# Performance work log

Hardware: AMD Instinct MI355X
Metric: run time of the kernel (lower is better)

Reference implementation:

```python
import jax, jax.numpy as jnp
import numpy as np

B, L, IN_DIM, D, H, NCONV = 64, 400, 500, 128, 8, 4
HD = D // H  # head dim = 16


def _conv1d(x, w, b, pad, groups=1):
    # x: [B, L, Cin], w: [k, Cin//groups, Cout]
    y = jax.lax.conv_general_dilated(
        x, w, window_strides=(1,), padding=[(pad, pad)],
        dimension_numbers=('NWC', 'WIO', 'NWC'), feature_group_count=groups)
    return y + b


def _layernorm(x, g, b, eps=1e-5):
    mu = jnp.mean(x, axis=-1, keepdims=True)
    var = jnp.mean(jnp.square(x - mu), axis=-1, keepdims=True)
    return (x - mu) * jax.lax.rsqrt(var + eps) * g + b


def _posenc(L, d):
    pos = jnp.arange(L, dtype=jnp.float32)[:, None]                 # [L,1]
    div = jnp.exp(jnp.arange(0, d, 2, dtype=jnp.float32) * (-jnp.log(10000.0) / d))
    ang = pos * div                                                 # [L, d/2]
    return jnp.stack([jnp.sin(ang), jnp.cos(ang)], axis=-1).reshape(L, d)


def setup_inputs() -> dict:
    key = jax.random.key(0)
    ks = jax.random.split(key, 24)
    s = lambda k, shape, scale: jax.random.normal(k, shape, dtype=jnp.float32) * scale
    inp = {
        'x': s(ks[0], (B, L, IN_DIM), 1.0),
        # init conv: k=5, 500 -> 128
        'w_init': s(ks[1], (5, IN_DIM, D), 0.02),
        'b_init': jnp.zeros((D,), jnp.float32),
        # 4 depthwise-separable conv layers (pre-LN, residual): depthwise k=7
        'ln_conv_g': jnp.ones((NCONV, D), jnp.float32),
        'ln_conv_b': jnp.zeros((NCONV, D), jnp.float32),
        'w_dw': s(ks[2], (NCONV, 7, 1, D), 0.1),
        'b_dw': jnp.zeros((NCONV, D), jnp.float32),
        'w_pw': s(ks[3], (NCONV, 1, D, D), 0.05),
        'b_pw': jnp.zeros((NCONV, D), jnp.float32),
        # self-attention (pre-LN, residual)
        'ln_att_g': jnp.ones((D,), jnp.float32),
        'ln_att_b': jnp.zeros((D,), jnp.float32),
        'wq': s(ks[4], (D, D), 0.05), 'bq': jnp.zeros((D,), jnp.float32),
        'wk': s(ks[5], (D, D), 0.05), 'bk': jnp.zeros((D,), jnp.float32),
        'wv': s(ks[6], (D, D), 0.05), 'bv': jnp.zeros((D,), jnp.float32),
        'wo': s(ks[7], (D, D), 0.05), 'bo': jnp.zeros((D,), jnp.float32),
        # FFN (pre-LN, residual)
        'ln_ffn_g': jnp.ones((D,), jnp.float32),
        'ln_ffn_b': jnp.zeros((D,), jnp.float32),
        'w1': s(ks[8], (D, D), 0.05), 'b1': jnp.zeros((D,), jnp.float32),
        'w2': s(ks[9], (D, D), 0.05), 'b2': jnp.zeros((D,), jnp.float32),
    }
    return inp


def reference(x, w_init, b_init, ln_conv_g, ln_conv_b, w_dw, b_dw, w_pw, b_pw,
              ln_att_g, ln_att_b, wq, bq, wk, bk, wv, bv, wo, bo,
              ln_ffn_g, ln_ffn_b, w1, b1, w2, b2):
    # 1) init conv (Conv1d k=5 pad=2, 500 -> 128); torch permutes, equivalent NWC conv
    h = _conv1d(x, w_init, b_init, pad=2)                    # [B, L, D]
    # 2) positional encoding
    h = h + _posenc(h.shape[1], D)
    for i in range(NCONV):
        res = h
        h = _layernorm(h, ln_conv_g[i], ln_conv_b[i])
        h = _conv1d(h, w_dw[i], b_dw[i], pad=3, groups=D)    # depthwise k=7
        h = _conv1d(h, w_pw[i], b_pw[i], pad=0)              # pointwise 1x1
        h = jax.nn.relu(h) + res
    # 4) multi-head self-attention, pre-LN + residual
    res = h
    hn = _layernorm(h, ln_att_g, ln_att_b)
    q = (hn @ wq + bq).reshape(B, L, H, HD)
    k = (hn @ wk + bk).reshape(B, L, H, HD)
    v = (hn @ wv + bv).reshape(B, L, H, HD)
    scores = jnp.einsum('bqhd,bkhd->bhqk', q, k) / jnp.sqrt(jnp.float32(HD))
    attn = jax.nn.softmax(scores, axis=-1)
    o = jnp.einsum('bhqk,bkhd->bqhd', attn, v).reshape(B, L, D)
    h = o @ wo + bo + res
    # 5) FFN, pre-LN + residual
    res = h
    hn = _layernorm(h, ln_ffn_g, ln_ffn_b)
    h = jax.nn.relu(hn @ w1 + b1) @ w2 + b2 + res
    return h
```

## Files before the change

kernel.cpp:

```cpp
#include <hip/hip_runtime.h>
#include <hip/hip_bf16.h>
#include <math.h>

#define B 64
#define L 400
#define IN_DIM 500
#define D 128
#define H 8
#define HD 16
#define NCONV 4
#define BL (B*L)

typedef __attribute__((ext_vector_type(8))) unsigned short ushort8;
typedef __attribute__((ext_vector_type(8))) short bf16x8;
typedef __attribute__((ext_vector_type(4))) float f32x4;

__device__ __forceinline__ unsigned short f2bf(float f) {
    unsigned u = __float_as_uint(f);
    unsigned r = (u + 0x7fffu + ((u >> 16) & 1u)) >> 16;
    return (unsigned short)r;
}
__device__ __forceinline__ float bf2f(unsigned short u) {
    return __uint_as_float(((unsigned)u) << 16);
}

__device__ __forceinline__ void gload16(const void* g, void* l) {
    __builtin_amdgcn_global_load_lds(
        (const __attribute__((address_space(1))) unsigned int*)g,
        (__attribute__((address_space(3))) unsigned int*)l,
        16, 0, 0);
}

__global__ __launch_bounds__(256) void k_cvt_x(
        const float* __restrict__ x, unsigned short* __restrict__ xb) {
    int idx = blockIdx.x * 256 + threadIdx.x;
    int row = idx >> 6, ch = idx & 63;
    int b = row / 404, rr = row - b * 404;
    ushort8 o = (ushort8)0;
    if (rr >= 2 && rr < 402) {
        int l = rr - 2;
        const float* src = x + ((size_t)b * 400 + l) * 500 + ch * 8;
        if (ch < 62) {
            float4 v0 = *(const float4*)(src);
            float4 v1 = *(const float4*)(src + 4);
            o[0] = f2bf(v0.x); o[1] = f2bf(v0.y); o[2] = f2bf(v0.z); o[3] = f2bf(v0.w);
            o[4] = f2bf(v1.x); o[5] = f2bf(v1.y); o[6] = f2bf(v1.z); o[7] = f2bf(v1.w);
        } else {
#pragma unroll
            for (int j = 0; j < 8; ++j) {
                int c = ch * 8 + j;
                o[j] = (c < 500) ? f2bf(src[j]) : (unsigned short)0;
            }
        }
    }
    *(ushort8*)(xb + (size_t)idx * 8) = o;
}

__global__ __launch_bounds__(256) void k_cvt_w(
        const float* __restrict__ w, unsigned short* __restrict__ wbt) {
    int idx = blockIdx.x * 256 + threadIdx.x;
    int k = idx & 511, n = (idx >> 9) & 127, t = idx >> 16;
    float v = (k < 500) ? w[((size_t)t * 500 + k) * 128 + n] : 0.f;
    wbt[idx] = f2bf(v);
}

__global__ __launch_bounds__(256) void k_cvt_wall(
        const float* w0, const float* w1, const float* w2, const float* w3,
        const float* w4, const float* w5, const float* w6, const float* w7,
        const float* w8, const float* w9, unsigned short* __restrict__ out) {
    const float* arr[10] = {w0,w1,w2,w3,w4,w5,w6,w7,w8,w9};
    int widx = blockIdx.x >> 6;
    const float* w = arr[widx];
    int idx = ((blockIdx.x & 63) << 8) + threadIdx.x;
    int n = idx >> 7, k = idx & 127;
    out[(size_t)widx * 16384 + idx] = f2bf(w[k * 128 + n]);
}

#define TM 80
#define BK 64
__global__ __launch_bounds__(256) void k_initconv_mfma(
        const unsigned short* __restrict__ xb,
        const unsigned short* __restrict__ wbt,
        const float* __restrict__ bias, float* __restrict__ out) {
    __shared__ unsigned short As[84 * BK];
    __shared__ unsigned short Ws[5][64 * BK];
    int tid = threadIdx.x;
    int b = blockIdx.x / 10;
    int rem = blockIdx.x - b * 10;
    int l0 = (rem >> 1) * TM;
    int nh = rem & 1;
    int lane = tid & 63, wave = tid >> 6;
    int kgrp = lane >> 4, lm = lane & 15;

    f32x4 acc[5];
#pragma unroll
    for (int mf = 0; mf < 5; ++mf) acc[mf] = (f32x4)0.f;

    const unsigned short* abase = xb + ((size_t)(b * 404 + l0)) * 512;
    const unsigned short* wbase = wbt + (size_t)nh * 64 * 512;

    for (int k0 = 0; k0 < 512; k0 += BK) {
        for (int idx = tid; idx < 672; idx += 256) {
            int r = idx >> 3, sc = idx & 7;
            gload16(abase + (size_t)r * 512 + k0 + ((sc ^ (r & 7)) * 8),
                    As + idx * 8);
        }
#pragma unroll
        for (int i = 0; i < 10; ++i) {
            int idx = tid + i * 256;
            int t = idx >> 9;
            int sub = idx & 511;
            int n = sub >> 3, sc = sub & 7;
            gload16(wbase + (size_t)t * 128 * 512 + (size_t)n * 512 + k0
                        + ((sc ^ (n & 7)) * 8),
                    &Ws[t][0] + sub * 8);
        }
        __syncthreads();
        int n16 = wave * 16 + lm;
#pragma unroll
        for (int ks = 0; ks < 2; ++ks) {
            int gc = ks * 4 + kgrp;
            bf16x8 bfr[5];
#pragma unroll
            for (int t = 0; t < 5; ++t)
                bfr[t] = *(const bf16x8*)(&Ws[t][0] + n16 * 64
                                          + ((gc ^ (n16 & 7)) * 8));
#pragma unroll
            for (int mf = 0; mf < 5; ++mf) {
#pragma unroll
                for (int t = 0; t < 5; ++t) {
                    int r = mf * 16 + lm + t;
                    bf16x8 af = *(const bf16x8*)(As + r * 64
                                                 + ((gc ^ (r & 7)) * 8));
                    acc[mf] = __builtin_amdgcn_mfma_f32_16x16x32_bf16(
                        af, bfr[t], acc[mf], 0, 0, 0);
                }
            }
        }
        __syncthreads();
    }

    {
        int n = nh * 64 + wave * 16 + lm;
        float bs = bias[n];
        float pbase = expf(-(float)(n & ~1) * (9.210340371976184f / 128.0f));
#pragma unroll
        for (int mf = 0; mf < 5; ++mf) {
#pragma unroll
            for (int r = 0; r < 4; ++r) {
                int l = l0 + mf * 16 + kgrp * 4 + r;
                float ang = (float)l * pbase;
                float pe = (n & 1) ? cosf(ang) : sinf(ang);
                out[((size_t)b * 400 + l) * 128 + n] = acc[mf][r] + bs + pe;
            }
        }
    }
}

#define CB_ROWS 38
__global__ __launch_bounds__(256) void k_convblock(
        const float* __restrict__ hin, float* __restrict__ hout,
        const float* __restrict__ lng, const float* __restrict__ lnb,
        const float* __restrict__ wdw, const float* __restrict__ bdw,
        const unsigned short* __restrict__ wpt, const float* __restrict__ bpw) {
    __shared__ unsigned short Ws[128 * 128];
    __shared__ unsigned short Ln[CB_ROWS * 128];
    __shared__ unsigned short Dw[32 * 128];
    int tid = threadIdx.x;
    int b = blockIdx.x / 13;
    int tile = blockIdx.x - b * 13;
    int l0 = tile * 32;
    int lv = (l0 + 32 <= L) ? 32 : (L - l0);
    int lane = tid & 63, wave = tid >> 6;
    int lm = lane & 15, kgrp = lane >> 4;

#pragma unroll
    for (int i = 0; i < 8; ++i) {
        int idx = tid + i * 256;
        int n = idx >> 4, sc = idx & 15;
        gload16(wpt + (size_t)n * 128 + ((sc ^ (n & 15)) * 8), Ws + idx * 8);
    }

    {
        float2 gg = *(const float2*)(lng + lane * 2);
        float2 bb = *(const float2*)(lnb + lane * 2);
#pragma unroll
        for (int ri = 0; ri < 10; ++ri) {
            int r = wave + ri * 4;
            if (r < CB_ROWS) {
                int gl = l0 - 3 + r;
                bool ok = (gl >= 0 && gl < L);
                float2 v = make_float2(0.f, 0.f);
                if (ok) v = *(const float2*)(hin + ((size_t)b * L + gl) * 128 + lane * 2);
                float s = v.x + v.y, q = v.x * v.x + v.y * v.y;
#pragma unroll
                for (int off = 32; off; off >>= 1) {
                    s += __shfl_xor(s, off);
                    q += __shfl_xor(q, off);
                }
                float mu  = s * (1.f / 128.f);
                float var = q * (1.f / 128.f) - mu * mu;
                float inv = rsqrtf(var + 1e-5f);
                unsigned pk = 0;
                if (ok) {
                    float ox = (v.x - mu) * inv * gg.x + bb.x;
                    float oy = (v.y - mu) * inv * gg.y + bb.y;
                    pk = (unsigned)f2bf(ox) | ((unsigned)f2bf(oy) << 16);
                }
                *(unsigned*)(Ln + r * 128 + lane * 2) = pk;
            }
        }
    }
    __syncthreads();

    {
        int d = tid & 127, half = tid >> 7;
        float wr[7];
#pragma unroll
        for (int t = 0; t < 7; ++t) wr[t] = wdw[t * 128 + d];
        float bs = bdw[d];
        float win[7];
#pragma unroll
        for (int t = 0; t < 6; ++t) win[t] = bf2f(Ln[(half * 16 + t) * 128 + d]);
#pragma unroll
        for (int lj = 0; lj < 16; ++lj) {
            int l = half * 16 + lj;
            win[6] = bf2f(Ln[(l + 6) * 128 + d]);
            float a = bs;
#pragma unroll
            for (int t = 0; t < 7; ++t) a = fmaf(win[t], wr[t], a);
#pragma unroll
            for (int t = 0; t < 6; ++t) win[t] = win[t + 1];
            Dw[l * 128 + ((d >> 3) ^ (l & 15)) * 8 + (d & 7)] = f2bf(a);
        }
    }
    __syncthreads();

    f32x4 acc[2][2];
#pragma unroll
    for (int mf = 0; mf < 2; ++mf)
#pragma unroll
        for (int nt = 0; nt < 2; ++nt) acc[mf][nt] = (f32x4)0.f;
#pragma unroll
    for (int kc = 0; kc < 4; ++kc) {
        int c = kc * 4 + kgrp;
        bf16x8 af[2];
#pragma unroll
        for (int mf = 0; mf < 2; ++mf) {
            int r = mf * 16 + lm;
            af[mf] = *(const bf16x8*)(Dw + r * 128 + (c ^ (r & 15)) * 8);
        }
#pragma unroll
        for (int nt = 0; nt < 2; ++nt) {
            int n = wave * 32 + nt * 16 + lm;
            bf16x8 bfv = *(const bf16x8*)(Ws + n * 128 + (c ^ (n & 15)) * 8);
#pragma unroll
            for (int mf = 0; mf < 2; ++mf)
                acc[mf][nt] = __builtin_amdgcn_mfma_f32_16x16x32_bf16(
                    af[mf], bfv, acc[mf][nt], 0, 0, 0);
        }
    }

#pragma unroll
    for (int nt = 0; nt < 2; ++nt) {
        int n = wave * 32 + nt * 16 + lm;
        float bsn = bpw[n];
#pragma unroll
        for (int mf = 0; mf < 2; ++mf) {
#pragma unroll
            for (int r = 0; r < 4; ++r) {
                int row = mf * 16 + kgrp * 4 + r;
                if (row < lv) {
                    size_t gi = ((size_t)b * L + l0 + row) * 128 + n;
                    hout[gi] = fmaxf(acc[mf][nt][r] + bsn, 0.f) + hin[gi];
                }
            }
        }
    }
}

__global__ __launch_bounds__(256) void k_ln_gemm(
        const float* __restrict__ h, const float* __restrict__ g,
        const float* __restrict__ bta, const unsigned short* __restrict__ wt0,
        int nw, const float* __restrict__ bias0, const float* __restrict__ bias1,
        const float* __restrict__ bias2, unsigned short* __restrict__ out0,
        unsigned short* __restrict__ out1, unsigned short* __restrict__ out2,
        float s0, int relu) {
    __shared__ unsigned short As[32 * 128];
    __shared__ unsigned short Ws[128 * 128];
    int tid = threadIdx.x;
    int m0 = blockIdx.x * 32;
    int lane = tid & 63, wave = tid >> 6;
    int lm = lane & 15, kgrp = lane >> 4;
    int wm = wave >> 1, wn = wave & 1;

#pragma unroll
    for (int i = 0; i < 8; ++i) {
        int idx = tid + i * 256;
        int n = idx >> 4, sc = idx & 15;
        gload16(wt0 + (size_t)n * 128 + ((sc ^ (n & 15)) * 8), Ws + idx * 8);
    }

    {
        float2 gg = *(const float2*)(g + lane * 2);
        float2 bb = *(const float2*)(bta + lane * 2);
#pragma unroll
        for (int ri = 0; ri < 8; ++ri) {
            int r = wave + ri * 4;
            float2 v = *(const float2*)(h + ((size_t)m0 + r) * 128 + lane * 2);
            float s = v.x + v.y, q = v.x * v.x + v.y * v.y;
#pragma unroll
            for (int off = 32; off; off >>= 1) {
                s += __shfl_xor(s, off);
                q += __shfl_xor(q, off);
            }
            float mu  = s * (1.f / 128.f);
            float var = q * (1.f / 128.f) - mu * mu;
            float inv = rsqrtf(var + 1e-5f);
            float ox = (v.x - mu) * inv * gg.x + bb.x;
            float oy = (v.y - mu) * inv * gg.y + bb.y;
            unsigned pk = (unsigned)f2bf(ox) | ((unsigned)f2bf(oy) << 16);
            *(unsigned*)(As + r * 128 + ((lane >> 2) ^ (r & 15)) * 8
                         + ((lane * 2) & 7)) = pk;
        }
    }

    for (int i = 0; i < nw; ++i) {
        __syncthreads();
        f32x4 acc[4];
#pragma unroll
        for (int nt = 0; nt < 4; ++nt) acc[nt] = (f32x4)0.f;
#pragma unroll
        for (int kc = 0; kc < 4; ++kc) {
            int c = kc * 4 + kgrp;
            int r = wm * 16 + lm;
            bf16x8 af = *(const bf16x8*)(As + r * 128 + (c ^ (r & 15)) * 8);
#pragma unroll
            for (int nt = 0; nt < 4; ++nt) {
                int n = wn * 64 + nt * 16 + lm;
                bf16x8 bfv = *(const bf16x8*)(Ws + n * 128 + (c ^ (n & 15)) * 8);
                acc[nt] = __builtin_amdgcn_mfma_f32_16x16x32_bf16(
                    af, bfv, acc[nt], 0, 0, 0);
            }
        }
        const float* bias = (i == 0) ? bias0 : (i == 1) ? bias1 : bias2;
        unsigned short* out = (i == 0) ? out0 : (i == 1) ? out1 : out2;
        float sc0 = (i == 0) ? s0 : 1.f;
#pragma unroll
        for (int nt = 0; nt < 4; ++nt) {
            int n = wn * 64 + nt * 16 + lm;
            float bsn = bias[n];
#pragma unroll
            for (int r = 0; r < 4; ++r) {
                size_t m = (size_t)m0 + wm * 16 + kgrp * 4 + r;
                float v = acc[nt][r] + bsn;
                if (relu) v = fmaxf(v, 0.f);
                out[m * 128 + n] = f2bf(v * sc0);
            }
        }
        if (i + 1 < nw) {
            __syncthreads();
            const unsigned short* wp = wt0 + (size_t)(i + 1) * 16384;
#pragma unroll
            for (int j = 0; j < 8; ++j) {
                int idx = tid + j * 256;
                int n = idx >> 4, sc = idx & 15;
                gload16(wp + (size_t)n * 128 + ((sc ^ (n & 15)) * 8), Ws + idx * 8);
            }
        }
    }
}

__global__ __launch_bounds__(256) void k_gemm_bf16(
        const unsigned short* __restrict__ A,
        const unsigned short* __restrict__ Wt,
        const float* __restrict__ bias,
        const float* __restrict__ res,
        float* __restrict__ outf,
        unsigned short* __restrict__ outb,
        int relu, float oscale) {
    __shared__ unsigned short As[32 * 128];
    __shared__ unsigned short Ws[128 * 128];
    int tid = threadIdx.x;
    int m0 = blockIdx.x * 32;
    int lane = tid & 63, wave = tid >> 6;
    int lm = lane & 15, kgrp = lane >> 4;
    int wm = wave >> 1, wn = wave & 1;

#pragma unroll
    for (int i = 0; i < 2; ++i) {
        int idx = tid + i * 256;
        int r = idx >> 4, sc = idx & 15;
        gload16(A + ((size_t)(m0 + r)) * 128 + ((sc ^ (r & 15)) * 8), As + idx * 8);
    }
#pragma unroll
    for (int i = 0; i < 8; ++i) {
        int idx = tid + i * 256;
        int n = idx >> 4, sc = idx & 15;
        gload16(Wt + ((size_t)n) * 128 + ((sc ^ (n & 15)) * 8), Ws + idx * 8);
    }
    __syncthreads();

    f32x4 acc[4];
#pragma unroll
    for (int nt = 0; nt < 4; ++nt) acc[nt] = (f32x4)0.f;

#pragma unroll
    for (int kc = 0; kc < 4; ++kc) {
        int c = kc * 4 + kgrp;
        int r = wm * 16 + lm;
        bf16x8 af = *(const bf16x8*)(As + (r * 16 + (c ^ (r & 15))) * 8);
#pragma unroll
        for (int nt = 0; nt < 4; ++nt) {
            int n = wn * 64 + nt * 16 + lm;
            bf16x8 bfv = *(const bf16x8*)(Ws + (n * 16 + (c ^ (n & 15))) * 8);
            acc[nt] = __builtin_amdgcn_mfma_f32_16x16x32_bf16(af, bfv, acc[nt], 0, 0, 0);
        }
    }

#pragma unroll
    for (int nt = 0; nt < 4; ++nt) {
        int n = wn * 64 + nt * 16 + lm;
        float bs = bias[n];
#pragma unroll
        for (int r = 0; r < 4; ++r) {
            size_t m = (size_t)m0 + wm * 16 + kgrp * 4 + r;
            float v = acc[nt][r] + bs;
            if (relu) v = fmaxf(v, 0.f);
            if (res)  v += res[m * 128 + n];
            if (outf) outf[m * 128 + n] = v;
            else      outb[m * 128 + n] = f2bf(v * oscale);
        }
    }
}

#define KS 40
#define VS 424
__global__ __launch_bounds__(256) void k_attn_mfma(
        const unsigned short* __restrict__ qb,
        const unsigned short* __restrict__ kb,
        const unsigned short* __restrict__ vb,
        unsigned short* __restrict__ out) {
    __shared__ __align__(16) unsigned short Kpad[400 * KS];
    __shared__ __align__(16) unsigned short Vt[16 * VS];
    __shared__ __align__(16) unsigned short Ptmp[4][16 * KS];
    int tid = threadIdx.x;
    int b = blockIdx.x >> 3, h = blockIdx.x & 7;
    int lane = tid & 63, wave = tid >> 6;
    int lm = lane & 15, kgrp = lane >> 4;

    for (int idx = tid; idx < 800; idx += 256) {
        int l = idx >> 1, half = idx & 1;
        ushort8 kv = *(const ushort8*)(kb + ((size_t)(b * 400 + l)) * 128 + h * 16 + half * 8);
        *(ushort8*)(Kpad + l * KS + half * 8) = kv;
        *(ushort8*)(Kpad + l * KS + 16 + half * 8) = (ushort8)0;
    }
    for (int idx = tid; idx < 800; idx += 256) {
        int kk = idx >> 1, dh = idx & 1;
        ushort8 vv = *(const ushort8*)(vb + ((size_t)(b * 400 + kk)) * 128 + h * 16 + dh * 8);
#pragma unroll
        for (int j = 0; j < 8; ++j) Vt[(dh * 8 + j) * VS + kk] = vv[j];
    }
    {
        int d = tid >> 4, kk = 400 + (tid & 15);
        Vt[d * VS + kk] = 0;
    }
    __syncthreads();

    unsigned short* Pw = Ptmp[wave];
    for (int tt = wave; tt < 25; tt += 4) {
        int q0 = tt * 16;
        bf16x8 Qf = *(const bf16x8*)(qb + ((size_t)(b * 400 + q0 + lm)) * 128 + h * 16 + kgrp * 8);
        f32x4 s[25];
#pragma unroll
        for (int kt = 0; kt < 25; ++kt) {
            bf16x8 Kf = *(const bf16x8*)(Kpad + (kt * 16 + lm) * KS + kgrp * 8);
            s[kt] = __builtin_amdgcn_mfma_f32_16x16x32_bf16(Qf, Kf, (f32x4)0.f, 0, 0, 0);
        }
        float rmax[4], rsum[4];
#pragma unroll
        for (int r = 0; r < 4; ++r) rmax[r] = -1e30f;
#pragma unroll
        for (int kt = 0; kt < 25; ++kt)
#pragma unroll
            for (int r = 0; r < 4; ++r) rmax[r] = fmaxf(rmax[r], s[kt][r]);
#pragma unroll
        for (int mask = 1; mask <= 8; mask <<= 1)
#pragma unroll
            for (int r = 0; r < 4; ++r) rmax[r] = fmaxf(rmax[r], __shfl_xor(rmax[r], mask));
#pragma unroll
        for (int r = 0; r < 4; ++r) rsum[r] = 0.f;
#pragma unroll
        for (int kt = 0; kt < 25; ++kt)
#pragma unroll
            for (int r = 0; r < 4; ++r) {
                float p = __expf(s[kt][r] - rmax[r]);
                s[kt][r] = p;
                rsum[r] += p;
            }
#pragma unroll
        for (int mask = 1; mask <= 8; mask <<= 1)
#pragma unroll
            for (int r = 0; r < 4; ++r) rsum[r] += __shfl_xor(rsum[r], mask);
        float rinv[4];
#pragma unroll
        for (int r = 0; r < 4; ++r) rinv[r] = 1.f / rsum[r];

        f32x4 O = (f32x4)0.f;
#pragma unroll
        for (int kc = 0; kc < 13; ++kc) {
#pragma unroll
            for (int t = 0; t < 2; ++t) {
                int kt = kc * 2 + t;
#pragma unroll
                for (int r = 0; r < 4; ++r) {
                    unsigned short pv = (kt < 25) ? f2bf(s[kt][r]) : (unsigned short)0;
                    Pw[(kgrp * 4 + r) * KS + t * 16 + lm] = pv;
                }
            }
            __builtin_amdgcn_wave_barrier();
            __builtin_amdgcn_s_waitcnt(0);
            __builtin_amdgcn_wave_barrier();
            bf16x8 Pf = *(const bf16x8*)(Pw + lm * KS + kgrp * 8);
            bf16x8 Vf = *(const bf16x8*)(Vt + lm * VS + kc * 32 + kgrp * 8);
            O = __builtin_amdgcn_mfma_f32_16x16x32_bf16(Pf, Vf, O, 0, 0, 0);
            __builtin_amdgcn_wave_barrier();
        }
#pragma unroll
        for (int r = 0; r < 4; ++r) {
            int q = q0 + kgrp * 4 + r;
            out[((size_t)(b * 400 + q)) * 128 + h * 16 + lm] = f2bf(O[r] * rinv[r]);
        }
    }
}

extern "C" void kernel_launch(void* const* d_in, const int* in_sizes, int n_in,
                              void* d_out, int out_size, void* d_ws, size_t ws_size,
                              hipStream_t stream) {
    (void)in_sizes; (void)n_in; (void)out_size; (void)ws_size;
    const float* x      = (const float*)d_in[0];
    const float* w_init = (const float*)d_in[1];
    const float* b_init = (const float*)d_in[2];
    const float* lncg   = (const float*)d_in[3];
    const float* lncb   = (const float*)d_in[4];
    const float* w_dw   = (const float*)d_in[5];
    const float* b_dw   = (const float*)d_in[6];
    const float* w_pw   = (const float*)d_in[7];
    const float* b_pw   = (const float*)d_in[8];
    const float* lnag   = (const float*)d_in[9];
    const float* lnab   = (const float*)d_in[10];
    const float* wq     = (const float*)d_in[11];
    const float* bq     = (const float*)d_in[12];
    const float* wk     = (const float*)d_in[13];
    const float* bk     = (const float*)d_in[14];
    const float* wv     = (const float*)d_in[15];
    const float* bv     = (const float*)d_in[16];
    const float* wo     = (const float*)d_in[17];
    const float* bo     = (const float*)d_in[18];
    const float* lnfg   = (const float*)d_in[19];
    const float* lnfb   = (const float*)d_in[20];
    const float* w1     = (const float*)d_in[21];
    const float* b1     = (const float*)d_in[22];
    const float* w2     = (const float*)d_in[23];
    const float* b2     = (const float*)d_in[24];

    float* ws = (float*)d_ws;
    const size_t NBL = (size_t)BL * D;
    float* h0 = ws;
    float* outp = (float*)d_out;

    unsigned short* hnb = (unsigned short*)(ws + NBL);
    unsigned short* t0b = hnb + NBL;
    unsigned short* qb  = t0b + NBL;
    unsigned short* kb  = qb + NBL;
    unsigned short* vb  = kb + NBL;
    unsigned short* wt  = vb + NBL;
    unsigned short* xb  = wt + 10 * 16384;
    unsigned short* wbt = xb + (size_t)64 * 404 * 512;
    float* h1 = (float*)(wbt + (size_t)5 * 128 * 512);

    k_cvt_x<<<6464, 256, 0, stream>>>(x, xb);
    k_cvt_w<<<1280, 256, 0, stream>>>(w_init, wbt);
    k_cvt_wall<<<640, 256, 0, stream>>>(
        w_pw, w_pw + 16384, w_pw + 2 * 16384, w_pw + 3 * 16384,
        wq, wk, wv, wo, w1, w2, wt);

    k_initconv_mfma<<<640, 256, 0, stream>>>(xb, wbt, b_init, h0);

    for (int i = 0; i < NCONV; ++i) {
        const float* hin = (i & 1) ? h1 : h0;
        float* hout      = (i & 1) ? h0 : h1;
        k_convblock<<<832, 256, 0, stream>>>(
            hin, hout, lncg + i * D, lncb + i * D,
            w_dw + (size_t)i * 7 * D, b_dw + i * D,
            wt + (size_t)i * 16384, b_pw + i * D);
    }

    k_ln_gemm<<<800, 256, 0, stream>>>(h0, lnag, lnab, wt + 4 * 16384, 3,
                                       bq, bk, bv, qb, kb, vb, 0.25f, 0);
    k_attn_mfma<<<512, 256, 0, stream>>>(qb, kb, vb, t0b);
    k_gemm_bf16<<<800, 256, 0, stream>>>(t0b, wt + 7 * 16384, bo, h0,
                                         h0, nullptr, 0, 1.f);

    k_ln_gemm<<<800, 256, 0, stream>>>(h0, lnfg, lnfb, wt + 8 * 16384, 1,
                                       b1, nullptr, nullptr,
                                       t0b, nullptr, nullptr, 1.f, 1);
    k_gemm_bf16<<<800, 256, 0, stream>>>(t0b, wt + 9 * 16384, b2, h0,
                                         outp, nullptr, 0, 1.f);
}
```

Before: 341.0 us.

## Restructure attention: transposed S MFMA, register P via shuffles, split query tiles

The attention kernel now computes K·Qᵀ so each lane holds scores for a single query column. Row max and sum then need only two cross-lane shuffles, and P is packed to bf16 with v_cvt_pk_bf16_f32 and redistributed to the PV MFMA operand layout with __shfl, replacing the per-wave LDS round trip and its barriers. The grid is doubled so each block handles half of the query tiles, which raises parallelism but makes every block reload K and V into LDS. s_setprio hints are added around the MFMA sections.

```diff
diff --git a/kernel.cpp b/kernel.cpp
--- a/kernel.cpp
+++ b/kernel.cpp
@@ -22,6 +22,11 @@
 }
 __device__ __forceinline__ float bf2f(unsigned short u) {
     return __uint_as_float(((unsigned)u) << 16);
+}
+__device__ __forceinline__ unsigned cvtpk_bf16(float lo, float hi) {
+    unsigned r;
+    asm("v_cvt_pk_bf16_f32 %0, %1, %2" : "=v"(r) : "v"(lo), "v"(hi));
+    return r;
 }
 
 __device__ __forceinline__ void gload16(const void* g, void* l) {
@@ -192,7 +197,8 @@
                 bool ok = (gl >= 0 && gl < L);
                 float2 v = make_float2(0.f, 0.f);
                 if (ok) v = *(const float2*)(hin + ((size_t)b * L + gl) * 128 + lane * 2);
-                float s = v.x + v.y, q = v.x * v.x + v.y * v.y;
+                float s = v.x + v.y;
+                float q = v.x * v.x + v.y * v.y;
 #pragma unroll
                 for (int off = 32; off; off >>= 1) {
                     s += __shfl_xor(s, off);
@@ -308,7 +314,8 @@
         for (int ri = 0; ri < 8; ++ri) {
             int r = wave + ri * 4;
             float2 v = *(const float2*)(h + ((size_t)m0 + r) * 128 + lane * 2);
-            float s = v.x + v.y, q = v.x * v.x + v.y * v.y;
+            float s = v.x + v.y;
+            float q = v.x * v.x + v.y * v.y;
 #pragma unroll
             for (int off = 32; off; off >>= 1) {
                 s += __shfl_xor(s, off);
@@ -443,17 +450,16 @@
         unsigned short* __restrict__ out) {
     __shared__ __align__(16) unsigned short Kpad[400 * KS];
     __shared__ __align__(16) unsigned short Vt[16 * VS];
-    __shared__ __align__(16) unsigned short Ptmp[4][16 * KS];
     int tid = threadIdx.x;
-    int b = blockIdx.x >> 3, h = blockIdx.x & 7;
+    int b = blockIdx.x >> 4, h = (blockIdx.x >> 1) & 7, half = blockIdx.x & 1;
     int lane = tid & 63, wave = tid >> 6;
-    int lm = lane & 15, kgrp = lane >> 4;
+    int lm = lane & 15, g = lane >> 4;
 
     for (int idx = tid; idx < 800; idx += 256) {
-        int l = idx >> 1, half = idx & 1;
-        ushort8 kv = *(const ushort8*)(kb + ((size_t)(b * 400 + l)) * 128 + h * 16 + half * 8);
-        *(ushort8*)(Kpad + l * KS + half * 8) = kv;
-        *(ushort8*)(Kpad + l * KS + 16 + half * 8) = (ushort8)0;
+        int l = idx >> 1, hf = idx & 1;
+        ushort8 kv = *(const ushort8*)(kb + ((size_t)(b * 400 + l)) * 128 + h * 16 + hf * 8);
+        *(ushort8*)(Kpad + l * KS + hf * 8) = kv;
+        *(ushort8*)(Kpad + l * KS + 16 + hf * 8) = (ushort8)0;
     }
     for (int idx = tid; idx < 800; idx += 256) {
         int kk = idx >> 1, dh = idx & 1;
@@ -467,69 +473,66 @@
     }
     __syncthreads();
 
-    unsigned short* Pw = Ptmp[wave];
-    for (int tt = wave; tt < 25; tt += 4) {
+    int tlo = half ? 12 : 0, thi = half ? 25 : 12;
+    for (int tt = tlo + wave; tt < thi; tt += 4) {
         int q0 = tt * 16;
-        bf16x8 Qf = *(const bf16x8*)(qb + ((size_t)(b * 400 + q0 + lm)) * 128 + h * 16 + kgrp * 8);
+        bf16x8 Qf = *(const bf16x8*)(qb + ((size_t)(b * 400 + q0 + lm)) * 128 + h * 16 + g * 8);
         f32x4 s[25];
+        __builtin_amdgcn_s_setprio(1);
 #pragma unroll
         for (int kt = 0; kt < 25; ++kt) {
-            bf16x8 Kf = *(const bf16x8*)(Kpad + (kt * 16 + lm) * KS + kgrp * 8);
-            s[kt] = __builtin_amdgcn_mfma_f32_16x16x32_bf16(Qf, Kf, (f32x4)0.f, 0, 0, 0);
-        }
-        float rmax[4], rsum[4];
-#pragma unroll
-        for (int r = 0; r < 4; ++r) rmax[r] = -1e30f;
-#pragma unroll
-        for (int kt = 0; kt < 25; ++kt)
-#pragma unroll
-            for (int r = 0; r < 4; ++r) rmax[r] = fmaxf(rmax[r], s[kt][r]);
-#pragma unroll
-        for (int mask = 1; mask <= 8; mask <<= 1)
-#pragma unroll
-            for (int r = 0; r < 4; ++r) rmax[r] = fmaxf(rmax[r], __shfl_xor(rmax[r], mask));
-#pragma unroll
-        for (int r = 0; r < 4; ++r) rsum[r] = 0.f;
-#pragma unroll
-        for (int kt = 0; kt < 25; ++kt)
-#pragma unroll
-            for (int r = 0; r < 4; ++r) {
-                float p = __expf(s[kt][r] - rmax[r]);
-                s[kt][r] = p;
-                rsum[r] += p;
-            }
-#pragma unroll
-        for (int mask = 1; mask <= 8; mask <<= 1)
-#pragma unroll
-            for (int r = 0; r < 4; ++r) rsum[r] += __shfl_xor(rsum[r], mask);
-        float rinv[4];
-#pragma unroll
-        for (int r = 0; r < 4; ++r) rinv[r] = 1.f / rsum[r];
+            bf16x8 Kf = *(const bf16x8*)(Kpad + (kt * 16 + lm) * KS + g * 8);
+            s[kt] = __builtin_amdgcn_mfma_f32_16x16x32_bf16(Kf, Qf, (f32x4)0.f, 0, 0, 0);
+        }
+        __builtin_amdgcn_s_setprio(0);
+        float m = -1e30f;
+#pragma unroll
+        for (int kt = 0; kt < 25; ++kt) {
+            m = fmaxf(m, fmaxf(fmaxf(s[kt][0], s[kt][1]),
+                               fmaxf(s[kt][2], s[kt][3])));
+        }
+        m = fmaxf(m, __shfl_xor(m, 16));
+        m = fmaxf(m, __shfl_xor(m, 32));
+        float sum = 0.f;
+        unsigned w0[25], w1[25];
+#pragma unroll
+        for (int kt = 0; kt < 25; ++kt) {
+            float p0 = __expf(s[kt][0] - m);
+            float p1 = __expf(s[kt][1] - m);
+            float p2 = __expf(s[kt][2] - m);
+            float p3 = __expf(s[kt][3] - m);
+            sum += (p0 + p1) + (p2 + p3);
+            w0[kt] = cvtpk_bf16(p0, p1);
+            w1[kt] = cvtpk_bf16(p2, p3);
+        }
+        sum += __shfl_xor(sum, 16);
+        sum += __shfl_xor(sum, 32);
+        float rinv = 1.f / sum;
 
         f32x4 O = (f32x4)0.f;
+        int srcA = lm + ((g & 1) << 5);
 #pragma unroll
         for (int kc = 0; kc < 13; ++kc) {
-#pragma unroll
-            for (int t = 0; t < 2; ++t) {
-                int kt = kc * 2 + t;
-#pragma unroll
-                for (int r = 0; r < 4; ++r) {
-                    unsigned short pv = (kt < 25) ? f2bf(s[kt][r]) : (unsigned short)0;
-                    Pw[(kgrp * 4 + r) * KS + t * 16 + lm] = pv;
-                }
-            }
-            __builtin_amdgcn_wave_barrier();
-            __builtin_amdgcn_s_waitcnt(0);
-            __builtin_amdgcn_wave_barrier();
-            bf16x8 Pf = *(const bf16x8*)(Pw + lm * KS + kgrp * 8);
-            bf16x8 Vf = *(const bf16x8*)(Vt + lm * VS + kc * 32 + kgrp * 8);
-            O = __builtin_amdgcn_mfma_f32_16x16x32_bf16(Pf, Vf, O, 0, 0, 0);
-            __builtin_amdgcn_wave_barrier();
+            unsigned a0 = w0[2 * kc], b0 = w1[2 * kc];
+            unsigned a1 = (2 * kc + 1 < 25) ? w0[2 * kc + 1] : 0u;
+            unsigned b1 = (2 * kc + 1 < 25) ? w1[2 * kc + 1] : 0u;
+            unsigned sel0 = (g >= 2) ? a1 : a0;
+            unsigned sel1 = (g >= 2) ? b1 : b0;
+            union { int u[4]; bf16x8 v; } pf;
+            pf.u[0] = __shfl((int)sel0, srcA);
+            pf.u[1] = __shfl((int)sel1, srcA);
+            pf.u[2] = __shfl((int)sel0, srcA + 16);
+            pf.u[3] = __shfl((int)sel1, srcA + 16);
+            bf16x8 Vf = *(const bf16x8*)(Vt + lm * VS + kc * 32 + g * 8);
+            __builtin_amdgcn_s_setprio(1);
+            O = __builtin_amdgcn_mfma_f32_16x16x32_bf16(pf.v, Vf, O, 0, 0, 0);
+            __builtin_amdgcn_s_setprio(0);
         }
 #pragma unroll
         for (int r = 0; r < 4; ++r) {
-            int q = q0 + kgrp * 4 + r;
-            out[((size_t)(b * 400 + q)) * 128 + h * 16 + lm] = f2bf(O[r] * rinv[r]);
+            float rq = __shfl(rinv, g * 4 + r);
+            int q = q0 + g * 4 + r;
+            out[((size_t)(b * 400 + q)) * 128 + h * 16 + lm] = f2bf(O[r] * rq);
         }
     }
 }
@@ -598,7 +601,7 @@
 
     k_ln_gemm<<<800, 256, 0, stream>>>(h0, lnag, lnab, wt + 4 * 16384, 3,
                                        bq, bk, bv, qb, kb, vb, 0.25f, 0);
-    k_attn_mfma<<<512, 256, 0, stream>>>(qb, kb, vb, t0b);
+    k_attn_mfma<<<1024, 256, 0, stream>>>(qb, kb, vb, t0b);
     k_gemm_bf16<<<800, 256, 0, stream>>>(t0b, wt + 7 * 16384, bo, h0,
                                          h0, nullptr, 0, 1.f);
 
```

After: 356.2 us. 4.4% more time.
